# Kernel tuning notes

Measured on AMD Instinct MI355X. Metric: run time of the kernel, lower is better.

Reference implementation:

```python
import jax, jax.numpy as jnp
import numpy as np

B, T, NG, NP = 128, 100, 4096, 512


def setup_inputs() -> dict:
    key = jax.random.key(0)
    ks = jax.random.split(key, 6)
    return {
        "v": jax.random.normal(ks[0], (B, T, 2), dtype=jnp.float32) * 0.1,
        "p0": jax.random.normal(ks[1], (B, NP), dtype=jnp.float32),
        # Linear(Np->Ng, bias=False): weight [Ng, Np]
        "W_enc": jax.random.normal(ks[2], (NG, NP), dtype=jnp.float32) / np.sqrt(NP),
        # nn.RNN weights: W_ih [Ng, 2], W_hh [Ng, Ng], bias=False
        "W_ih": jax.random.normal(ks[3], (NG, 2), dtype=jnp.float32) / np.sqrt(2.0),
        "W_hh": jax.random.normal(ks[4], (NG, NG), dtype=jnp.float32) / np.sqrt(NG),
        # Linear(Ng->Np, bias=True): weight [Np, Ng], bias [Np]
        "W_dec": jax.random.normal(ks[5], (NP, NG), dtype=jnp.float32) / np.sqrt(NG),
        "b_dec": jnp.zeros((NP,), dtype=jnp.float32),
    }


def reference(v, p0, W_enc, W_ih, W_hh, W_dec, b_dec):
    # init hidden state: encoder(p0)  -> [B, Ng]
    h0 = p0 @ W_enc.T
    # precompute input projection for all steps: [T, B, Ng]
    vin = jnp.einsum('bti,gi->tbg', v, W_ih)

    def step(h, x_t):
        h_new = jnp.tanh(x_t + h @ W_hh.T)  # Elman tanh cell, bias=False
        return h_new, h_new

    _, g = jax.lax.scan(step, h0, vin)      # g: [T, B, Ng]
    g = jnp.swapaxes(g, 0, 1)               # [B, T, Ng]
    # decoder: place cell predictions [B, T, Np]
    place_preds = g @ W_dec.T + b_dec
    return place_preds
```

## Files before the change

kernel.cpp:

```cpp
#include <hip/hip_runtime.h>
#include <stdint.h>

namespace {
constexpr int kT = 100;
constexpr int kNG = 4096;
constexpr int kNP = 512;

__device__ __forceinline__ uint16_t f2bf(float f) {
  uint32_t u = __float_as_uint(f);
  u += 0x7FFFu + ((u >> 16) & 1u);
  return (uint16_t)(u >> 16);
}

__device__ __forceinline__ float fast_tanh(float x) {
  float xc = fminf(fmaxf(x, -15.f), 15.f);
  float e = __expf(2.f * xc);
  return (e - 1.f) / (e + 1.f);
}

__device__ __forceinline__ void gl2lds16(const void* g, void* l) {
  __builtin_amdgcn_global_load_lds((const __attribute__((address_space(1))) unsigned int*)g,
                                   (__attribute__((address_space(3))) unsigned int*)l, 16, 0, 0);
}

__device__ __forceinline__ size_t a_img_off(int b, int g) {
  return ((size_t)(((g >> 7) * 8 + (b >> 4)) * 4 + ((g >> 5) & 3)) * 64 +
          ((g >> 3) & 3) * 16 + (b & 15)) * 8 + (g & 7);
}
}

typedef short bf16x8 __attribute__((ext_vector_type(8)));
typedef float f32x4 __attribute__((ext_vector_type(4)));

__global__ __launch_bounds__(512) void cvt_whh_kernel(const float* __restrict__ W,
                                                      uint16_t* __restrict__ WhS,
                                                      int* __restrict__ flags) {
  if (blockIdx.x == 4095) {
    for (int i = threadIdx.x; i < 2048; i += 512) flags[i] = 0;
  }
  const int idx = blockIdx.x * 512 + threadIdx.x;
  const int g = idx >> 9;
  const int k0 = (idx & 511) << 3;
  const float4 x = *(const float4*)(W + (size_t)g * kNG + k0);
  const float4 y = *(const float4*)(W + (size_t)g * kNG + k0 + 4);
  uint4 u;
  u.x = (uint32_t)f2bf(x.x) | ((uint32_t)f2bf(x.y) << 16);
  u.y = (uint32_t)f2bf(x.z) | ((uint32_t)f2bf(x.w) << 16);
  u.z = (uint32_t)f2bf(y.x) | ((uint32_t)f2bf(y.y) << 16);
  u.w = (uint32_t)f2bf(y.z) | ((uint32_t)f2bf(y.w) << 16);
  const int gt = g >> 7, c = g & 127;
  const int nt = c >> 4, col = c & 15;
  const int chunk = k0 >> 7, ktl = (k0 >> 5) & 3, half = (k0 >> 3) & 3;
  const size_t off = ((size_t)(((gt * 32 + chunk) * 8 + nt) * 4 + ktl) * 64 + half * 16 + col) * 8;
  *(uint4*)(WhS + off) = u;
}

__global__ __launch_bounds__(512) void cvt_wdec_kernel(const float* __restrict__ W,
                                                       uint16_t* __restrict__ WdS) {
  const int idx = blockIdx.x * 512 + threadIdx.x;
  const int p = idx >> 9;
  const int k0 = (idx & 511) << 3;
  const float4 x = *(const float4*)(W + (size_t)p * kNG + k0);
  const float4 y = *(const float4*)(W + (size_t)p * kNG + k0 + 4);
  uint4 u;
  u.x = (uint32_t)f2bf(x.x) | ((uint32_t)f2bf(x.y) << 16);
  u.y = (uint32_t)f2bf(x.z) | ((uint32_t)f2bf(x.w) << 16);
  u.z = (uint32_t)f2bf(y.x) | ((uint32_t)f2bf(y.y) << 16);
  u.w = (uint32_t)f2bf(y.z) | ((uint32_t)f2bf(y.w) << 16);
  const int pt = p >> 7, c = p & 127;
  const int nt = c >> 4, col = c & 15;
  const int chunk = k0 >> 7, ktl = (k0 >> 5) & 3, half = (k0 >> 3) & 3;
  const size_t off = ((size_t)(((pt * 32 + chunk) * 8 + nt) * 4 + ktl) * 64 + half * 16 + col) * 8;
  *(uint4*)(WdS + off) = u;
}

__global__ __launch_bounds__(512, 2) void enc_kernel(const float* __restrict__ p0,
                                                     const float* __restrict__ Wenc,
                                                     uint16_t* __restrict__ H0S) {
  __shared__ alignas(16) uint16_t Wlds[16 * 64 * 8];
  const int tid = threadIdx.x;
  const int g0 = blockIdx.x * 16;
  for (int f = tid; f < 16 * 64; f += 512) {
    const int kt = f >> 6, fl = f & 63;
    const int g = g0 + (fl & 15);
    const int k = kt * 32 + ((fl >> 4) << 3);
    const float* s = Wenc + (size_t)g * kNP + k;
    uint16_t* d = Wlds + f * 8;
#pragma unroll
    for (int j = 0; j < 8; j++) d[j] = f2bf(s[j]);
  }
  __syncthreads();
  const int wave = tid >> 6;
  const int lane = tid & 63;
  const int mrow = wave * 16 + (lane & 15);
  const float* arow = p0 + (size_t)mrow * kNP + ((lane >> 4) << 3);
  f32x4 acc = {0.f, 0.f, 0.f, 0.f};
#pragma unroll
  for (int kt = 0; kt < 16; kt++) {
    const float* ap = arow + kt * 32;
    bf16x8 a;
#pragma unroll
    for (int j = 0; j < 8; j++) a[j] = (short)f2bf(ap[j]);
    bf16x8 b = *(const bf16x8*)(Wlds + (kt * 64 + lane) * 8);
    acc = __builtin_amdgcn_mfma_f32_16x16x32_bf16(a, b, acc, 0, 0, 0);
  }
  const int gcol = g0 + (lane & 15);
  const int rbase = wave * 16 + ((lane >> 4) << 2);
#pragma unroll
  for (int r = 0; r < 4; r++) {
    H0S[a_img_off(rbase + r, gcol)] = f2bf(acc[r]);
  }
}

__global__ __launch_bounds__(512, 2) void rnn_loop_kernel(const uint16_t* __restrict__ WhS,
                                                          const uint16_t* __restrict__ H0S,
                                                          uint16_t* __restrict__ Gsw,
                                                          float* __restrict__ Part,
                                                          const float* __restrict__ v,
                                                          const float* __restrict__ Wih,
                                                          int* __restrict__ flags) {
  extern __shared__ uint16_t wlds[];
  const int tid = threadIdx.x;
  const int wave = tid >> 6, lane = tid & 63;
  const int bid = blockIdx.x;
  const int xcd = bid & 7;
  const int gt = xcd * 4 + (bid >> 6);
  const int ks = (bid >> 3) & 7;
  const int mg = wave >> 1, ng = wave & 1;

  int* pcnt = flags;
  int* hcnt = flags + 32 * 32;

  {
    const uint16_t* src = WhS + ((size_t)gt << 19) + ((size_t)(ks * 4) << 14);
#pragma unroll
    for (int i = 0; i < 16; i++) {
      const int j = wave * 16 + i;
      gl2lds16(src + (j << 9) + (lane << 3), (void*)(wlds + (j << 9)));
    }
  }
  __syncthreads();

  const int rbred = ks * 16 + (tid >> 5);
  const int gl = (tid & 31) << 2;
  const int gg = gt * 128 + gl;
  float* myPart = Part + (((size_t)(gt * 8 + ks)) << 14);

  for (int t = 0; t < kT; t++) {
    if (t > 0) {
      const int target = 8 * t;
      if (tid < 5) {
        int* f = (tid < 4) ? (hcnt + ((ks * 4 + tid) << 5)) : (hcnt + (gt << 5));
        while (__hip_atomic_load(f, __ATOMIC_RELAXED, __HIP_MEMORY_SCOPE_AGENT) < target)
          __builtin_amdgcn_s_sleep(1);
      }
      __builtin_amdgcn_fence(__ATOMIC_ACQUIRE, "workgroup");
      __syncthreads();
    }

    const uint16_t* Aimg = (t == 0) ? H0S : (Gsw + (((size_t)(t - 1)) << 19));
    f32x4 acc[2][4];
#pragma unroll
    for (int i = 0; i < 2; i++)
#pragma unroll
      for (int j = 0; j < 4; j++) acc[i][j] = (f32x4){0.f, 0.f, 0.f, 0.f};

#pragma unroll
    for (int kc = 0; kc < 4; kc++) {
      const uint16_t* Ac = Aimg + ((size_t)(ks * 4 + kc) << 14);
      bf16x8 a[2][4];
#pragma unroll
      for (int mi = 0; mi < 2; mi++)
#pragma unroll
        for (int ktl = 0; ktl < 4; ktl++)
          a[mi][ktl] = *(const bf16x8*)(Ac + ((((mg * 2 + mi) * 4 + ktl) * 64 + lane) << 3));
#pragma unroll
      for (int ktl = 0; ktl < 4; ktl++) {
#pragma unroll
        for (int nt = 0; nt < 4; nt++) {
          bf16x8 b = *(const bf16x8*)(wlds + (kc << 14) +
                                      ((((ng * 4 + nt) * 4 + ktl) * 64 + lane) << 3));
          acc[0][nt] = __builtin_amdgcn_mfma_f32_16x16x32_bf16(a[0][ktl], b, acc[0][nt], 0, 0, 0);
          acc[1][nt] = __builtin_amdgcn_mfma_f32_16x16x32_bf16(a[1][ktl], b, acc[1][nt], 0, 0, 0);
        }
      }
    }
    {
      const int gcol0 = (ng << 6);
      const int rbase = (mg << 5) + ((lane >> 4) << 2);
#pragma unroll
      for (int mi = 0; mi < 2; mi++)
#pragma unroll
        for (int nt = 0; nt < 4; nt++)
#pragma unroll
          for (int r = 0; r < 4; r++) {
            const int b = rbase + (mi << 4) + r;
            const int g = gcol0 + (nt << 4) + (lane & 15);
            myPart[(b << 7) + g] = acc[mi][nt][r];
          }
    }
    asm volatile("s_waitcnt vmcnt(0)" ::: "memory");
    __syncthreads();
    if (tid == 0) {
      __hip_atomic_fetch_add(pcnt + (gt << 5), 1, __ATOMIC_RELAXED, __HIP_MEMORY_SCOPE_AGENT);
      const int tgt = 8 * (t + 1);
      while (__hip_atomic_load(pcnt + (gt << 5), __ATOMIC_RELAXED, __HIP_MEMORY_SCOPE_AGENT) < tgt)
        __builtin_amdgcn_s_sleep(1);
      __builtin_amdgcn_fence(__ATOMIC_ACQUIRE, "workgroup");
    }
    __syncthreads();

    {
      const float* pb = Part + (((size_t)(gt * 8)) << 14) + (rbred << 7) + gl;
      f32x4 pv[8];
#pragma unroll
      for (int j = 0; j < 8; j++) {
        asm volatile("global_load_dwordx4 %0, %1, off sc0"
                     : "=v"(pv[j])
                     : "v"(pb + ((size_t)j << 14))
                     : "memory");
      }
      asm volatile("s_waitcnt vmcnt(0)" ::: "memory");
      __builtin_amdgcn_sched_barrier(0);
      float s0 = 0.f, s1 = 0.f, s2 = 0.f, s3 = 0.f;
#pragma unroll
      for (int j = 0; j < 8; j++) {
        s0 += pv[j][0]; s1 += pv[j][1]; s2 += pv[j][2]; s3 += pv[j][3];
      }
      const float v0 = v[(rbred * kT + t) * 2 + 0];
      const float v1 = v[(rbred * kT + t) * 2 + 1];
      const float4 w0 = *(const float4*)(Wih + gg * 2);
      const float4 w1 = *(const float4*)(Wih + gg * 2 + 4);
      const uint16_t h0 = f2bf(fast_tanh(s0 + v0 * w0.x + v1 * w0.y));
      const uint16_t h1 = f2bf(fast_tanh(s1 + v0 * w0.z + v1 * w0.w));
      const uint16_t h2 = f2bf(fast_tanh(s2 + v0 * w1.x + v1 * w1.y));
      const uint16_t h3 = f2bf(fast_tanh(s3 + v0 * w1.z + v1 * w1.w));
      const uint32_t lo = (uint32_t)h0 | ((uint32_t)h1 << 16);
      const uint32_t hi = (uint32_t)h2 | ((uint32_t)h3 << 16);
      const unsigned long long uval = ((unsigned long long)hi << 32) | lo;
      uint16_t* Gt = Gsw + (((size_t)t) << 19);
      __hip_atomic_exchange((unsigned long long*)(Gt + a_img_off(rbred, gg)), uval,
                            __ATOMIC_RELAXED, __HIP_MEMORY_SCOPE_AGENT);
    }
    asm volatile("s_waitcnt vmcnt(0)" ::: "memory");
    __syncthreads();
    if (tid == 0)
      __hip_atomic_fetch_add(hcnt + (gt << 5), 1, __ATOMIC_RELAXED, __HIP_MEMORY_SCOPE_AGENT);
  }
}

__global__ __launch_bounds__(512, 4) void stepmm_kernel(const uint16_t* __restrict__ Asrc,
                                                        const uint16_t* __restrict__ WhS,
                                                        float* __restrict__ Part) {
  __shared__ alignas(16) uint16_t lds[32768];
  const int tid = threadIdx.x;
  const int wave = tid >> 6, lane = tid & 63;
  const int gt = blockIdx.x >> 3, ks = blockIdx.x & 7;
  const int mg = wave >> 1, ng = wave & 1;
  const uint16_t* Wbase = WhS + ((size_t)gt << 19);
  f32x4 acc[2][4];
#pragma unroll
  for (int i = 0; i < 2; i++)
#pragma unroll
    for (int j = 0; j < 4; j++) acc[i][j] = (f32x4){0.f, 0.f, 0.f, 0.f};

  for (int kc = 0; kc < 4; kc++) {
    const int chunk = ks * 4 + kc;
    const uint16_t* Ac = Asrc + ((size_t)chunk << 14);
    const uint16_t* Bc = Wbase + ((size_t)chunk << 14);
#pragma unroll
    for (int i = 0; i < 8; i++) {
      const int j = wave * 8 + i;
      const uint16_t* s = (j < 32) ? (Ac + (j << 9)) : (Bc + ((j - 32) << 9));
      gl2lds16(s + (lane << 3), (void*)(lds + (j << 9)));
    }
    __syncthreads();
    const uint16_t* lA = lds;
    const uint16_t* lB = lds + 16384;
#pragma unroll
    for (int ktl = 0; ktl < 4; ktl++) {
      bf16x8 a0 = *(const bf16x8*)(lA + ((((mg * 2 + 0) * 4 + ktl) * 64 + lane) << 3));
      bf16x8 a1 = *(const bf16x8*)(lA + ((((mg * 2 + 1) * 4 + ktl) * 64 + lane) << 3));
#pragma unroll
      for (int nt = 0; nt < 4; nt++) {
        bf16x8 b = *(const bf16x8*)(lB + ((((ng * 4 + nt) * 4 + ktl) * 64 + lane) << 3));
        acc[0][nt] = __builtin_amdgcn_mfma_f32_16x16x32_bf16(a0, b, acc[0][nt], 0, 0, 0);
        acc[1][nt] = __builtin_amdgcn_mfma_f32_16x16x32_bf16(a1, b, acc[1][nt], 0, 0, 0);
      }
    }
    __syncthreads();
  }
  const int g0 = (gt << 7) + (ng << 6);
  const int rb = (mg << 5) + ((lane >> 4) << 2);
#pragma unroll
  for (int mi = 0; mi < 2; mi++)
#pragma unroll
    for (int nt = 0; nt < 4; nt++)
#pragma unroll
      for (int r = 0; r < 4; r++) {
        const int b = rb + (mi << 4) + r;
        const int g = g0 + (nt << 4) + (lane & 15);
        Part[(((size_t)(ks * 128 + b)) << 12) + g] = acc[mi][nt][r];
      }
}

__global__ __launch_bounds__(256) void steptanh_kernel(const float* __restrict__ Part,
                                                       const float* __restrict__ v,
                                                       const float* __restrict__ Wih,
                                                       uint16_t* __restrict__ Gt, int t) {
  const int tg = blockIdx.x * 256 + threadIdx.x;
  const int b = tg >> 9;
  const int g0 = (tg & 511) << 3;
  float s[8];
#pragma unroll
  for (int j = 0; j < 8; j++) s[j] = 0.f;
#pragma unroll
  for (int ks = 0; ks < 8; ks++) {
    const float4* p = (const float4*)(Part + (((size_t)(ks * 128 + b)) << 12) + g0);
    const float4 x = p[0], y = p[1];
    s[0] += x.x; s[1] += x.y; s[2] += x.z; s[3] += x.w;
    s[4] += y.x; s[5] += y.y; s[6] += y.z; s[7] += y.w;
  }
  const float v0 = v[(b * kT + t) * 2 + 0];
  const float v1 = v[(b * kT + t) * 2 + 1];
  uint16_t h[8];
#pragma unroll
  for (int j = 0; j < 8; j++) {
    const int g = g0 + j;
    const float pre = s[j] + v0 * Wih[g * 2 + 0] + v1 * Wih[g * 2 + 1];
    h[j] = f2bf(fast_tanh(pre));
  }
  uint4 u;
  u.x = (uint32_t)h[0] | ((uint32_t)h[1] << 16);
  u.y = (uint32_t)h[2] | ((uint32_t)h[3] << 16);
  u.z = (uint32_t)h[4] | ((uint32_t)h[5] << 16);
  u.w = (uint32_t)h[6] | ((uint32_t)h[7] << 16);
  const size_t off = ((size_t)(((g0 >> 7) * 8 + (b >> 4)) * 4 + ((g0 >> 5) & 3)) * 64 +
                      ((g0 >> 3) & 3) * 16 + (b & 15)) * 8;
  *(uint4*)(Gt + off) = u;
}

__global__ __launch_bounds__(512, 4) void dec_kernel(const uint16_t* __restrict__ Gsw,
                                                     const uint16_t* __restrict__ WdS,
                                                     const float* __restrict__ bd,
                                                     float* __restrict__ out) {
  __shared__ alignas(16) uint16_t lds[32768];
  const int tid = threadIdx.x;
  const int wave = tid >> 6, lane = tid & 63;
  const int t = blockIdx.x >> 2, pt = blockIdx.x & 3;
  const int mg = wave >> 1, ng = wave & 1;
  const uint16_t* Abase = Gsw + (size_t)t * 524288;
  const uint16_t* Bbase = WdS + (size_t)pt * 524288;
  f32x4 acc[2][4];
#pragma unroll
  for (int i = 0; i < 2; i++)
#pragma unroll
    for (int j = 0; j < 4; j++) acc[i][j] = (f32x4){0.f, 0.f, 0.f, 0.f};

  for (int chunk = 0; chunk < 32; chunk++) {
    const uint16_t* Ac = Abase + ((size_t)chunk << 14);
    const uint16_t* Bc = Bbase + ((size_t)chunk << 14);
#pragma unroll
    for (int i = 0; i < 8; i++) {
      const int j = wave * 8 + i;
      const uint16_t* s = (j < 32) ? (Ac + (j << 9)) : (Bc + ((j - 32) << 9));
      gl2lds16(s + (lane << 3), (void*)(lds + (j << 9)));
    }
    __syncthreads();
    const uint16_t* lA = lds;
    const uint16_t* lB = lds + 16384;
#pragma unroll
    for (int ktl = 0; ktl < 4; ktl++) {
      bf16x8 a0 = *(const bf16x8*)(lA + ((((mg * 2 + 0) * 4 + ktl) * 64 + lane) << 3));
      bf16x8 a1 = *(const bf16x8*)(lA + ((((mg * 2 + 1) * 4 + ktl) * 64 + lane) << 3));
#pragma unroll
      for (int nt = 0; nt < 4; nt++) {
        bf16x8 b = *(const bf16x8*)(lB + ((((ng * 4 + nt) * 4 + ktl) * 64 + lane) << 3));
        acc[0][nt] = __builtin_amdgcn_mfma_f32_16x16x32_bf16(a0, b, acc[0][nt], 0, 0, 0);
        acc[1][nt] = __builtin_amdgcn_mfma_f32_16x16x32_bf16(a1, b, acc[1][nt], 0, 0, 0);
      }
    }
    __syncthreads();
  }
  const int p0c = (pt << 7) + (ng << 6);
  const int rb = (mg << 5) + ((lane >> 4) << 2);
#pragma unroll
  for (int mi = 0; mi < 2; mi++)
#pragma unroll
    for (int nt = 0; nt < 4; nt++) {
      const int p = p0c + (nt << 4) + (lane & 15);
      const float bias = bd[p];
#pragma unroll
      for (int r = 0; r < 4; r++) {
        const int b = rb + (mi << 4) + r;
        out[((size_t)b * kT + t) * kNP + p] = acc[mi][nt][r] + bias;
      }
    }
}

extern "C" void kernel_launch(void* const* d_in, const int* in_sizes, int n_in,
                              void* d_out, int out_size, void* d_ws, size_t ws_size,
                              hipStream_t stream) {
  const float* v    = (const float*)d_in[0];
  const float* p0   = (const float*)d_in[1];
  const float* Wenc = (const float*)d_in[2];
  const float* Wih  = (const float*)d_in[3];
  const float* Whh  = (const float*)d_in[4];
  const float* Wdec = (const float*)d_in[5];
  const float* bdec = (const float*)d_in[6];
  float* out = (float*)d_out;

  uint8_t* ws = (uint8_t*)d_ws;
  uint16_t* WhS = (uint16_t*)(ws);
  uint16_t* WdS = (uint16_t*)(ws + 33554432);
  uint16_t* H0S = (uint16_t*)(ws + 37748736);
  uint16_t* Gsw = (uint16_t*)(ws + 38797312);
  float*    Part = (float*)(ws + 143654912);
  int*      flags = (int*)(ws + 160432128);

  cvt_whh_kernel<<<4096, 512, 0, stream>>>(Whh, WhS, flags);
  cvt_wdec_kernel<<<512, 512, 0, stream>>>(Wdec, WdS);
  enc_kernel<<<256, 512, 0, stream>>>(p0, Wenc, H0S);

  const uint16_t* WhS_c = WhS;
  const uint16_t* H0S_c = H0S;
  void* args[7] = {(void*)&WhS_c, (void*)&H0S_c, (void*)&Gsw, (void*)&Part,
                   (void*)&v, (void*)&Wih, (void*)&flags};
  hipError_t e = hipLaunchCooperativeKernel(rnn_loop_kernel, dim3(256), dim3(512), args,
                                            (unsigned int)131072, stream);
  if (e != hipSuccess) {
    (void)hipGetLastError();
    for (int t = 0; t < kT; t++) {
      const uint16_t* Asrc = (t == 0) ? H0S : (Gsw + (size_t)(t - 1) * 524288);
      stepmm_kernel<<<256, 512, 0, stream>>>(Asrc, WhS, Part);
      steptanh_kernel<<<256, 256, 0, stream>>>(Part, v, Wih, Gsw + (size_t)t * 524288, t);
    }
  }

  dec_kernel<<<400, 512, 0, stream>>>(Gsw, WdS, bdec, out);
}
```

Baseline: 1.151 ms.

## Replace shared atomic counters with per-block timestamp flags and hoist invariant loads

Swaps the contended fetch_add counters (one per group, hit by 8 blocks) for per-block timestamp slots written with atomic exchange. Waiting blocks now poll several flags in parallel across threads, and all 8 lanes wait on the partial-sum barrier instead of one thread. It also hoists the W_ih and v loads out of the critical path and replaces the sc0 loads with a buffer_inv followed by plain loads. The intent is to cut atomic contention and barrier latency in the recurrent loop, at the cost of more polling threads and a cache invalidate each step. The flags buffer layout changes, so it must be zeroed to match.

```diff
diff --git a/kernel.cpp b/kernel.cpp
--- a/kernel.cpp
+++ b/kernel.cpp
@@ -128,8 +128,8 @@
   const int ks = (bid >> 3) & 7;
   const int mg = wave >> 1, ng = wave & 1;
 
-  int* pcnt = flags;
-  int* hcnt = flags + 32 * 32;
+  int* pstamp = flags;
+  int* hstamp = flags + 256;
 
   {
     const uint16_t* src = WhS + ((size_t)gt << 19) + ((size_t)(ks * 4) << 14);
@@ -146,17 +146,24 @@
   const int gg = gt * 128 + gl;
   float* myPart = Part + (((size_t)(gt * 8 + ks)) << 14);
 
+  const float4 w0 = *(const float4*)(Wih + gg * 2);
+  const float4 w1 = *(const float4*)(Wih + gg * 2 + 4);
+
   for (int t = 0; t < kT; t++) {
     if (t > 0) {
-      const int target = 8 * t;
-      if (tid < 5) {
-        int* f = (tid < 4) ? (hcnt + ((ks * 4 + tid) << 5)) : (hcnt + (gt << 5));
-        while (__hip_atomic_load(f, __ATOMIC_RELAXED, __HIP_MEMORY_SCOPE_AGENT) < target)
+      if (tid < 40) {
+        const int idx = (tid < 32) ? ((ks * 4 + (tid >> 3)) * 8 + (tid & 7))
+                                   : (gt * 8 + (tid - 32));
+        int* f = hstamp + idx;
+        while (__hip_atomic_load(f, __ATOMIC_RELAXED, __HIP_MEMORY_SCOPE_AGENT) < t)
           __builtin_amdgcn_s_sleep(1);
       }
       __builtin_amdgcn_fence(__ATOMIC_ACQUIRE, "workgroup");
       __syncthreads();
     }
+
+    const float v0 = v[(rbred * kT + t) * 2 + 0];
+    const float v1 = v[(rbred * kT + t) * 2 + 1];
 
     const uint16_t* Aimg = (t == 0) ? H0S : (Gsw + (((size_t)(t - 1)) << 19));
     f32x4 acc[2][4];
@@ -201,36 +208,29 @@
     }
     asm volatile("s_waitcnt vmcnt(0)" ::: "memory");
     __syncthreads();
-    if (tid == 0) {
-      __hip_atomic_fetch_add(pcnt + (gt << 5), 1, __ATOMIC_RELAXED, __HIP_MEMORY_SCOPE_AGENT);
-      const int tgt = 8 * (t + 1);
-      while (__hip_atomic_load(pcnt + (gt << 5), __ATOMIC_RELAXED, __HIP_MEMORY_SCOPE_AGENT) < tgt)
+    if (tid == 0)
+      __hip_atomic_exchange(pstamp + gt * 8 + ks, t + 1, __ATOMIC_RELAXED,
+                            __HIP_MEMORY_SCOPE_AGENT);
+    if (tid < 8) {
+      while (__hip_atomic_load(pstamp + gt * 8 + tid, __ATOMIC_RELAXED,
+                               __HIP_MEMORY_SCOPE_AGENT) < t + 1)
         __builtin_amdgcn_s_sleep(1);
-      __builtin_amdgcn_fence(__ATOMIC_ACQUIRE, "workgroup");
-    }
-    __syncthreads();
+    }
+    __builtin_amdgcn_fence(__ATOMIC_ACQUIRE, "workgroup");
+    __syncthreads();
+
+    asm volatile("buffer_inv sc0\n\ts_waitcnt vmcnt(0)" ::: "memory");
 
     {
       const float* pb = Part + (((size_t)(gt * 8)) << 14) + (rbred << 7) + gl;
       f32x4 pv[8];
 #pragma unroll
-      for (int j = 0; j < 8; j++) {
-        asm volatile("global_load_dwordx4 %0, %1, off sc0"
-                     : "=v"(pv[j])
-                     : "v"(pb + ((size_t)j << 14))
-                     : "memory");
-      }
-      asm volatile("s_waitcnt vmcnt(0)" ::: "memory");
-      __builtin_amdgcn_sched_barrier(0);
+      for (int j = 0; j < 8; j++) pv[j] = *(const f32x4*)(pb + ((size_t)j << 14));
       float s0 = 0.f, s1 = 0.f, s2 = 0.f, s3 = 0.f;
 #pragma unroll
       for (int j = 0; j < 8; j++) {
         s0 += pv[j][0]; s1 += pv[j][1]; s2 += pv[j][2]; s3 += pv[j][3];
       }
-      const float v0 = v[(rbred * kT + t) * 2 + 0];
-      const float v1 = v[(rbred * kT + t) * 2 + 1];
-      const float4 w0 = *(const float4*)(Wih + gg * 2);
-      const float4 w1 = *(const float4*)(Wih + gg * 2 + 4);
       const uint16_t h0 = f2bf(fast_tanh(s0 + v0 * w0.x + v1 * w0.y));
       const uint16_t h1 = f2bf(fast_tanh(s1 + v0 * w0.z + v1 * w0.w));
       const uint16_t h2 = f2bf(fast_tanh(s2 + v0 * w1.x + v1 * w1.y));
@@ -245,7 +245,8 @@
     asm volatile("s_waitcnt vmcnt(0)" ::: "memory");
     __syncthreads();
     if (tid == 0)
-      __hip_atomic_fetch_add(hcnt + (gt << 5), 1, __ATOMIC_RELAXED, __HIP_MEMORY_SCOPE_AGENT);
+      __hip_atomic_exchange(hstamp + gt * 8 + ks, t + 1, __ATOMIC_RELAXED,
+                            __HIP_MEMORY_SCOPE_AGENT);
   }
 }
 
```

After: 1.352 ms. +17.5%, slower.
